# Kernel tuning notes

Hardware: AMD Instinct MI355X
Metric: run time of the kernel (lower is better)

The kernel has to match this reference:

```python
import math
import jax, jax.numpy as jnp
import numpy as np

NUM_HEADS = 16
NUM_BUCKETS = 32
MAX_DISTANCE = 128
NEG_INF = -1e9
LN_EPS = 1e-5


def _rel_pos_bias(rab_emb, T):
    # buckets for relative position (i - j) clamped at 0, T5-style log buckets
    i = jnp.arange(T)[:, None]
    j = jnp.arange(T)[None, :]
    n = jnp.clip(i - j, 0, None)  # = -(mem - ctx), clamped min 0
    max_exact = NUM_BUCKETS // 2
    large = max_exact + (
        jnp.log(n.astype(jnp.float32) / max_exact + 1e-6)
        / math.log(MAX_DISTANCE / max_exact)
        * (NUM_BUCKETS - max_exact)
    ).astype(jnp.int32)
    large = jnp.minimum(large, NUM_BUCKETS - 1)
    buckets = jnp.where(n < max_exact, n, large)  # [T, T]
    return rab_emb[buckets].transpose(2, 0, 1)[None]  # [1, H, T, T]


def setup_inputs() -> dict:
    key = jax.random.key(0)
    ks = jax.random.split(key, 8)
    B, T, D = 2, 1024, 1024
    x = jax.random.normal(ks[0], (B, T, D), dtype=jnp.float32)
    # additive causal mask: 0 where allowed, -1e9 where blocked (code tests ==0 for allowed)
    causal_block = jnp.triu(jnp.ones((T, T), dtype=bool), k=1)
    attention_mask = jnp.where(causal_block, NEG_INF, 0.0).astype(jnp.float32)
    # key padding: second sequence has last 256 positions padded
    lengths = jnp.array([T, T - 256])
    key_padding_mask = jnp.arange(T)[None, :] >= lengths[:, None]  # True = pad
    s = 1.0 / math.sqrt(D)
    W_in = jax.random.normal(ks[1], (4 * D, D), dtype=jnp.float32) * s
    b_in = jax.random.normal(ks[2], (4 * D,), dtype=jnp.float32) * 0.02
    W_out = jax.random.normal(ks[3], (D, D), dtype=jnp.float32) * s
    b_out = jax.random.normal(ks[4], (D,), dtype=jnp.float32) * 0.02
    gamma = jnp.ones((D,), dtype=jnp.float32)
    beta = jnp.zeros((D,), dtype=jnp.float32)
    rab_emb = jax.random.normal(ks[5], (NUM_BUCKETS, NUM_HEADS), dtype=jnp.float32) * 0.02
    return {
        "x": x,
        "attention_mask": attention_mask,
        "key_padding_mask": key_padding_mask,
        "W_in": W_in,
        "b_in": b_in,
        "W_out": W_out,
        "b_out": b_out,
        "gamma": gamma,
        "beta": beta,
        "rab_emb": rab_emb,
    }


def reference(x, attention_mask, key_padding_mask, W_in, b_in, W_out, b_out, gamma, beta, rab_emb):
    B, T, D = x.shape
    H = NUM_HEADS
    hd = D // H
    alpha = hd ** (-0.5)

    h = jax.nn.silu(x @ W_in.T + b_in)  # [B, T, 4D]
    U, V, Q, K = jnp.split(h, 4, axis=-1)

    def heads(t):
        return t.reshape(B, T, H, hd).transpose(0, 2, 1, 3)  # [B, H, T, hd]

    Qh, Kh, Vh = heads(Q), heads(K), heads(V)

    rab = _rel_pos_bias(rab_emb, T)  # [1, H, T, T]
    logits = jnp.einsum("bhtd,bhsd->bhts", Qh, Kh) * alpha + rab + attention_mask[None, None]

    valid = (~key_padding_mask).astype(jnp.float32)[:, None, None, :]  # [B,1,1,T]
    allowed = (attention_mask == 0).astype(jnp.float32)[None, None] * valid  # [B,1,T,T] bcast
    # padded keys: torch masked_fill(-inf) then logits_safe -> -1e9
    logits = jnp.where(valid == 0, NEG_INF, logits)

    denom = jnp.clip(jnp.sum(allowed, axis=-1, keepdims=True), 1.0, None)
    attention = jax.nn.silu(logits) / denom  # pointwise SiLU attention, no softmax

    AV = jnp.einsum("bhts,bhsd->bthd", attention, Vh).reshape(B, T, D)

    mu = jnp.mean(AV, axis=-1, keepdims=True)
    var = jnp.var(AV, axis=-1, keepdims=True)
    normed = (AV - mu) / jnp.sqrt(var + LN_EPS) * gamma + beta

    y = (normed * U) @ W_out.T + b_out  # U_flat == U (head reshape round-trips)
    return x + y
```

## Files before the change

### kernel.cpp

```cpp
#include <hip/hip_runtime.h>
#include <stdint.h>

#define DEV static __device__ __forceinline__

typedef unsigned short u16;
typedef float floatx4 __attribute__((ext_vector_type(4)));
typedef short bf16x8 __attribute__((ext_vector_type(8)));
typedef unsigned short ushort8v __attribute__((ext_vector_type(8)));

constexpr int Tn = 1024;
constexpr int Dn = 1024;
constexpr int Hn = 16;
constexpr int FD = 4096;

DEV float b2f(u16 u) { union { unsigned int i; float f; } v; v.i = ((unsigned int)u) << 16; return v.f; }
DEV u16 f2b(float f) {
  union { float f; unsigned int i; } v; v.f = f;
  unsigned int x = v.i;
  x += 0x7fffu + ((x >> 16) & 1u);
  return (u16)(x >> 16);
}

DEV void async16(const void* g, void* l) {
  __builtin_amdgcn_global_load_lds((const __attribute__((address_space(1))) void*)g,
                                   (__attribute__((address_space(3))) void*)l,
                                   16, 0, 0);
}

DEV bool is_bf16(const unsigned* gdet) { return gdet[0] == 0x3F803F80u; }
DEV int kp_mode(const unsigned* kp) {
  unsigned d511 = kp[511];
  if (d511 == 0x01010101u) return 1;
  unsigned d1023 = kp[1023];
  if (d1023 == 0x3F803F80u) return 2;
  unsigned d2047 = kp[2047];
  return (d2047 == 0x3F800000u) ? 3 : 0;
}
DEV int nchunks(int qt) { return (qt < 6) ? 1 : ((qt < 12) ? 2 : 3); }

__global__ void cvt_big(const void* __restrict__ x, const void* __restrict__ wi,
                        const void* __restrict__ wo, u16* __restrict__ xb,
                        u16* __restrict__ wib, u16* __restrict__ wob,
                        const unsigned* __restrict__ gdet)
{
  if (is_bf16(gdet)) return;
  int i0 = blockIdx.x * 256 + threadIdx.x;
#pragma unroll
  for (int k = 0; k < 4; k++) {
    int i = i0 + k * 458752;
    const void* src; u16* dst; int j;
    if (i < 524288)       { src = x;  dst = xb;  j = i; }
    else if (i < 1572864) { src = wi; dst = wib; j = i - 524288; }
    else                  { src = wo; dst = wob; j = i - 1572864; }
    float4 v = ((const float4*)src)[j];
    ushort4 o; o.x = f2b(v.x); o.y = f2b(v.y); o.z = f2b(v.z); o.w = f2b(v.w);
    ((ushort4*)dst)[j] = o;
  }
}

__global__ void cvt_small(const void* __restrict__ bi, const void* __restrict__ bo,
                          const void* __restrict__ ga, const void* __restrict__ be,
                          float* __restrict__ smallf)
{
  const bool fbf = is_bf16((const unsigned*)ga);
  int i = blockIdx.x * 256 + threadIdx.x;
  if (i >= 7168) return;
  const void* src; int j;
  if (i < 4096)      { src = bi; j = i; }
  else if (i < 5120) { src = bo; j = i - 4096; }
  else if (i < 6144) { src = ga; j = i - 5120; }
  else               { src = be; j = i - 6144; }
  smallf[i] = fbf ? b2f(((const u16*)src)[j]) : ((const float*)src)[j];
}

__global__ void prep2_kern(const void* __restrict__ kp, const void* __restrict__ rab,
                           const unsigned* __restrict__ gdet,
                           float* __restrict__ biasG, float* __restrict__ denomG,
                           unsigned long long* __restrict__ kmaskG)
{
  const int tid = threadIdx.x;
  if (blockIdx.x == 2) {
    const bool fbf = is_bf16(gdet);
    for (int i = tid; i < Hn * Tn; i += 256) {
      int hh = i >> 10, d = i & 1023;
      int bk;
      if (d < 16) bk = d;
      else {
        float lg = logf((float)d * 0.0625f + 1e-6f) / logf(8.f) * 16.f;
        bk = 16 + (int)lg;
        bk = bk < 31 ? bk : 31;
      }
      int j = bk * Hn + hh;
      biasG[i] = fbf ? b2f(((const u16*)rab)[j]) : ((const float*)rab)[j];
    }
    return;
  }
  const int b = blockIdx.x;
  const int mode = kp_mode((const unsigned*)kp);
  __shared__ unsigned char vb[1024];
  __shared__ int wtot[4];
  int vv[4];
  const int t0 = tid * 4;
#pragma unroll
  for (int i = 0; i < 4; i++) {
    int t = b * Tn + t0 + i;
    int pad;
    if (mode == 0)      pad = (((const int*)kp)[t] != 0);
    else if (mode == 1) pad = (((const unsigned char*)kp)[t] != 0);
    else if (mode == 2) pad = (((const u16*)kp)[t] != 0);
    else                pad = (((const float*)kp)[t] != 0.f);
    vv[i] = pad ? 0 : 1;
    vb[t0 + i] = (unsigned char)vv[i];
  }
  int p1 = vv[0], p2 = p1 + vv[1], p3 = p2 + vv[2], p4 = p3 + vv[3];
  const int lane = tid & 63, w = tid >> 6;
  int ws = p4;
#pragma unroll
  for (int off = 1; off < 64; off <<= 1) {
    int t = __shfl_up(ws, off, 64);
    if (lane >= off) ws += t;
  }
  if (lane == 63) wtot[w] = ws;
  __syncthreads();
  int base = 0;
  for (int j = 0; j < w; j++) base += wtot[j];
  int excl = base + ws - p4;
  int c1 = excl + p1, c2 = excl + p2, c3 = excl + p3, c4 = excl + p4;
  denomG[b * Tn + t0 + 0] = (float)(c1 < 1 ? 1 : c1);
  denomG[b * Tn + t0 + 1] = (float)(c2 < 1 ? 1 : c2);
  denomG[b * Tn + t0 + 2] = (float)(c3 < 1 ? 1 : c3);
  denomG[b * Tn + t0 + 3] = (float)(c4 < 1 ? 1 : c4);
  if (tid < 16) {
    unsigned long long m = 0;
    for (int j = 0; j < 64; j++) m |= (unsigned long long)vb[tid * 64 + j] << j;
    kmaskG[b * 16 + tid] = m;
  }
}

template<int BM, int BN, int WR, int WC, int EPI>
__global__ __launch_bounds__(WR * WC * 64, 2)
void gemm_bt(const u16* __restrict__ Ac, const u16* __restrict__ Ar,
             const u16* __restrict__ Bc, const u16* __restrict__ Br,
             const float* __restrict__ biasf, void* __restrict__ C,
             const unsigned* __restrict__ gdet, int M, int N, int K)
{
  constexpr int NT = WR * WC * 64;
  __shared__ u16 As[BM * 32];
  __shared__ u16 Bs[BN * 32];
  const int fbf = is_bf16(gdet) ? 1 : 0;
  const u16* A  = fbf ? Ar : Ac;
  const u16* Bm = fbf ? Br : Bc;
  const int tid = threadIdx.x;
  const int lane = tid & 63;
  const int w = tid >> 6;
  const int wm = w / WC, wn = w % WC;
  const int q = lane >> 4, l16 = lane & 15;
  const int rowBase = blockIdx.y * BM;
  const int colBase = blockIdx.x * BN;
  const int ksl = K / gridDim.z;
  const int kb0 = blockIdx.z * ksl;

  floatx4 acc[4][4];
#pragma unroll
  for (int i = 0; i < 4; i++)
#pragma unroll
    for (int j = 0; j < 4; j++)
#pragma unroll
      for (int r = 0; r < 4; r++) acc[i][j][r] = 0.f;

  for (int kb = kb0; kb < kb0 + ksl; kb += 32) {
    __syncthreads();
#pragma unroll
    for (int i = 0; i < BM * 4 / NT; i++) {
      int c = i * NT + tid;
      async16(&A[(size_t)(rowBase + (c >> 2)) * K + kb + (c & 3) * 8], &As[c * 8]);
    }
#pragma unroll
    for (int i = 0; i < BN * 4 / NT; i++) {
      int c = i * NT + tid;
      async16(&Bm[(size_t)(colBase + (c >> 2)) * K + kb + (c & 3) * 8], &Bs[c * 8]);
    }
    __syncthreads();
    bf16x8 af[4], bfr[4];
#pragma unroll
    for (int mt = 0; mt < 4; mt++)
      af[mt] = *(const bf16x8*)&As[(wm * 64 + mt * 16 + l16) * 32 + q * 8];
#pragma unroll
    for (int nt = 0; nt < 4; nt++)
      bfr[nt] = *(const bf16x8*)&Bs[(wn * 64 + nt * 16 + l16) * 32 + q * 8];
#pragma unroll
    for (int mt = 0; mt < 4; mt++)
#pragma unroll
      for (int nt = 0; nt < 4; nt++)
        acc[mt][nt] = __builtin_amdgcn_mfma_f32_16x16x32_bf16(af[mt], bfr[nt], acc[mt][nt], 0, 0, 0);
  }

  const size_t pOff = (size_t)blockIdx.z * M * N;
#pragma unroll
  for (int mt = 0; mt < 4; mt++)
#pragma unroll
    for (int nt = 0; nt < 4; nt++) {
      int col = colBase + wn * 64 + nt * 16 + l16;
      float bcol = (EPI == 0) ? biasf[col] : 0.f;
#pragma unroll
      for (int r = 0; r < 4; r++) {
        int row = rowBase + wm * 64 + mt * 16 + q * 4 + r;
        size_t idx = (size_t)row * N + col;
        float v = acc[mt][nt][r] + bcol;
        if (EPI == 0) {
          v = v / (1.f + __expf(-v));
          ((u16*)C)[idx] = f2b(v);
        } else {
          ((float*)C)[pOff + idx] = v;
        }
      }
    }
}

__global__ __launch_bounds__(256)
void reduce2(const float* __restrict__ Gp, const void* __restrict__ X,
             const float* __restrict__ bout, void* __restrict__ out,
             const unsigned* __restrict__ gdet)
{
  const int fbf = is_bf16(gdet) ? 1 : 0;
  const int row = blockIdx.x;
  const int tid = threadIdx.x;
  const size_t ridx = (size_t)row * Dn;
  float4 a = ((const float4*)(Gp + ridx))[tid];
#pragma unroll
  for (int ks = 1; ks < 4; ks++) {
    float4 p = ((const float4*)(Gp + (size_t)ks * 2097152 + ridx))[tid];
    a.x += p.x; a.y += p.y; a.z += p.z; a.w += p.w;
  }
  float4 bb = ((const float4*)bout)[tid];
  a.x += bb.x; a.y += bb.y; a.z += bb.z; a.w += bb.w;
  if (fbf) {
    ushort4 xv = ((const ushort4*)X)[ridx / 4 + tid];
    a.x += b2f(xv.x); a.y += b2f(xv.y); a.z += b2f(xv.z); a.w += b2f(xv.w);
    ushort4 o; o.x = f2b(a.x); o.y = f2b(a.y); o.z = f2b(a.z); o.w = f2b(a.w);
    ((ushort4*)out)[ridx / 4 + tid] = o;
  } else {
    float4 xv = ((const float4*)X)[ridx / 4 + tid];
    a.x += xv.x; a.y += xv.y; a.z += xv.z; a.w += xv.w;
    ((float4*)out)[ridx / 4 + tid] = a;
  }
}

__global__ __launch_bounds__(256)
void vt_kern(const u16* __restrict__ h, u16* __restrict__ VtG)
{
  __shared__ u16 L[4096];
  const int tid = threadIdx.x;
  const int tt = blockIdx.x, head = blockIdx.y, b = blockIdx.z;
  const u16* hb = h + (size_t)b * Tn * FD;
#pragma unroll
  for (int i = 0; i < 2; i++) {
    int s = i * 256 + tid;
    async16(&hb[(size_t)(tt * 64 + (s >> 3)) * FD + 1024 + head * 64 + (s & 7) * 8], &L[s * 8]);
  }
  __syncthreads();
  u16* vout = VtG + ((size_t)(b * Hn + head)) * 64 * Tn;
#pragma unroll
  for (int i = 0; i < 2; i++) {
    int oc = i * 256 + tid;
    int d = oc >> 3, tc = oc & 7;
    ushort8v v;
#pragma unroll
    for (int j = 0; j < 8; j++) v[j] = L[(tc * 8 + j) * 64 + d];
    *(ushort8v*)&vout[(size_t)d * Tn + tt * 64 + tc * 8] = v;
  }
}

__global__ __launch_bounds__(256, 4)
void attn_kern(const u16* __restrict__ h, const u16* __restrict__ VtG,
               const float* __restrict__ biasG, const float* __restrict__ denomG,
               const unsigned long long* __restrict__ kmaskG,
               float* __restrict__ AV)
{
  __shared__ u16 Qs[4096];
  __shared__ u16 Ks[4096];
  __shared__ u16 Vs[4096];
  __shared__ u16 Ps[4096];
  __shared__ float biasL[1024];
  const int tid = threadIdx.x;
  const int lane = tid & 63;
  const int w = tid >> 6;
  const int q = lane >> 4, l16 = lane & 15;

  int qt = 0, rem = blockIdx.x;
  for (;;) { int P = nchunks(qt); if (rem < P) break; rem -= P; qt++; }
  const int c = rem;
  const int P = nchunks(qt);
  const int n = qt + 1, cb = n / P, cr = n % P;
  const int kt0 = c * cb + (c < cr ? c : cr);
  const int kt1 = kt0 + cb + (c < cr ? 1 : 0);

  const int head = blockIdx.y, b = blockIdx.z;
  const u16* hb = h + (size_t)b * Tn * FD;
  const u16* vtb = VtG + ((size_t)(b * Hn + head)) * 64 * Tn;

#pragma unroll
  for (int i = 0; i < 2; i++) {
    int s = i * 256 + tid;
    int row = s >> 3, dc = (s & 7) ^ (row & 7);
    async16(&hb[(size_t)(qt * 64 + row) * FD + 2048 + head * 64 + dc * 8], &Qs[s * 8]);
    async16(&hb[(size_t)(kt0 * 64 + row) * FD + 3072 + head * 64 + dc * 8], &Ks[s * 8]);
    async16(&vtb[(size_t)row * Tn + kt0 * 64 + dc * 8], &Vs[s * 8]);
  }
  async16(&biasG[head * Tn + tid * 4], &biasL[tid * 4]);
  __syncthreads();

  const int sw0 = q ^ (l16 & 7);
  const int qrow = w * 16 + l16;
  bf16x8 bq0 = *(const bf16x8*)&Qs[(qrow * 8 + sw0) * 8];
  bf16x8 bq1 = *(const bf16x8*)&Qs[(qrow * 8 + (sw0 ^ 4)) * 8];
  const float dinv = 1.f / denomG[b * Tn + qt * 64 + qrow];

  floatx4 o[4];
#pragma unroll
  for (int nt = 0; nt < 4; nt++)
#pragma unroll
    for (int r = 0; r < 4; r++) o[nt][r] = 0.f;

  for (int kt = kt0; kt < kt1; kt++) {
    const unsigned long long km = kmaskG[b * 16 + kt];
    const int dq = (qt - kt) * 64 + qrow;
#pragma unroll
    for (int st = 0; st < 4; st++) {
      int rk = (st * 16 + l16) * 8;
      bf16x8 ak0 = *(const bf16x8*)&Ks[(rk + sw0) * 8];
      bf16x8 ak1 = *(const bf16x8*)&Ks[(rk + (sw0 ^ 4)) * 8];
      floatx4 sT;
#pragma unroll
      for (int r = 0; r < 4; r++) sT[r] = 0.f;
      sT = __builtin_amdgcn_mfma_f32_16x16x32_bf16(ak0, bq0, sT, 0, 0, 0);
      sT = __builtin_amdgcn_mfma_f32_16x16x32_bf16(ak1, bq1, sT, 0, 0, 0);
      unsigned mb = (unsigned)(km >> (st * 16 + q * 4)) & 0xFu;
      u16 pr[4];
#pragma unroll
      for (int r = 0; r < 4; r++) {
        int delta = dq - (st * 16 + q * 4 + r);
        float p = 0.f;
        if (((mb >> r) & 1u) && delta >= 0) {
          float xv = sT[r] * 0.125f + biasL[delta];
          p = xv * dinv / (1.f + __expf(-xv));
        }
        pr[r] = f2b(p);
      }
      unsigned lo = pr[0] | ((unsigned)pr[1] << 16);
      unsigned hi = pr[2] | ((unsigned)pr[3] << 16);
      int cch = (st * 2 + (q >> 1)) ^ (l16 & 7);
      *(uint2*)&Ps[w * 1024 + l16 * 64 + cch * 8 + (q & 1) * 4] = make_uint2(lo, hi);
    }
    int rp = w * 1024 + l16 * 64;
    bf16x8 ap0 = *(const bf16x8*)&Ps[rp + sw0 * 8];
    bf16x8 ap1 = *(const bf16x8*)&Ps[rp + (sw0 ^ 4) * 8];
#pragma unroll
    for (int nt = 0; nt < 4; nt++) {
      int rv = (nt * 16 + l16) * 8;
      bf16x8 bv0 = *(const bf16x8*)&Vs[(rv + sw0) * 8];
      bf16x8 bv1 = *(const bf16x8*)&Vs[(rv + (sw0 ^ 4)) * 8];
      o[nt] = __builtin_amdgcn_mfma_f32_16x16x32_bf16(ap0, bv0, o[nt], 0, 0, 0);
      o[nt] = __builtin_amdgcn_mfma_f32_16x16x32_bf16(ap1, bv1, o[nt], 0, 0, 0);
    }
    if (kt + 1 < kt1) {
      __syncthreads();
#pragma unroll
      for (int i = 0; i < 2; i++) {
        int s = i * 256 + tid;
        int row = s >> 3, dc = (s & 7) ^ (row & 7);
        async16(&hb[(size_t)((kt + 1) * 64 + row) * FD + 3072 + head * 64 + dc * 8], &Ks[s * 8]);
        async16(&vtb[(size_t)row * Tn + (kt + 1) * 64 + dc * 8], &Vs[s * 8]);
      }
      __syncthreads();
    }
  }

  float* avp = AV + (size_t)c * 2097152
             + ((size_t)b * Tn + qt * 64 + w * 16 + q * 4) * Dn + head * 64;
#pragma unroll
  for (int nt = 0; nt < 4; nt++)
#pragma unroll
    for (int r = 0; r < 4; r++)
      avp[(size_t)r * Dn + nt * 16 + l16] = o[nt][r];
}

__global__ __launch_bounds__(256)
void ln_mul(const float* __restrict__ AV, const u16* __restrict__ h,
            const float* __restrict__ gam, const float* __restrict__ bet,
            u16* __restrict__ z)
{
  struct alignas(8) U4 { u16 a, b, c, d; };
  const int row = blockIdx.x;
  const int tid = threadIdx.x;
  const int P = nchunks(row >> 6 & 15);
  float4 v = ((const float4*)(AV + (size_t)row * Dn))[tid];
  if (P > 1) {
    float4 p = ((const float4*)(AV + 2097152 + (size_t)row * Dn))[tid];
    v.x += p.x; v.y += p.y; v.z += p.z; v.w += p.w;
  }
  if (P > 2) {
    float4 p = ((const float4*)(AV + 4194304 + (size_t)row * Dn))[tid];
    v.x += p.x; v.y += p.y; v.z += p.z; v.w += p.w;
  }
  float s  = v.x + v.y + v.z + v.w;
  float s2 = v.x * v.x + v.y * v.y + v.z * v.z + v.w * v.w;
#pragma unroll
  for (int off = 32; off > 0; off >>= 1) {
    s  += __shfl_down(s, off, 64);
    s2 += __shfl_down(s2, off, 64);
  }
  __shared__ float red[8];
  const int lane = tid & 63, w = tid >> 6;
  if (lane == 0) { red[w] = s; red[4 + w] = s2; }
  __syncthreads();
  const float su = red[0] + red[1] + red[2] + red[3];
  const float sq = red[4] + red[5] + red[6] + red[7];
  const float mu = su * (1.f / 1024.f);
  const float var = sq * (1.f / 1024.f) - mu * mu;
  const float rstd = rsqrtf(var + 1e-5f);

  const U4 uu = ((const U4*)(h + (size_t)row * FD))[tid];
  const float4 g4 = ((const float4*)gam)[tid];
  const float4 b4 = ((const float4*)bet)[tid];
  float r0 = ((v.x - mu) * rstd * g4.x + b4.x) * b2f(uu.a);
  float r1 = ((v.y - mu) * rstd * g4.y + b4.y) * b2f(uu.b);
  float r2 = ((v.z - mu) * rstd * g4.z + b4.z) * b2f(uu.c);
  float r3 = ((v.w - mu) * rstd * g4.w + b4.w) * b2f(uu.d);
  U4 outv; outv.a = f2b(r0); outv.b = f2b(r1); outv.c = f2b(r2); outv.d = f2b(r3);
  ((U4*)(z + (size_t)row * Dn))[tid] = outv;
}

extern "C" void kernel_launch(void* const* d_in, const int* in_sizes, int n_in,
                              void* d_out, int out_size, void* d_ws, size_t ws_size,
                              hipStream_t stream)
{
  const void* x     = d_in[0];
  const void* kp    = d_in[2];
  const void* W_in  = d_in[3];
  const void* b_in  = d_in[4];
  const void* W_out = d_in[5];
  const void* b_out = d_in[6];
  const void* gamma = d_in[7];
  const void* beta  = d_in[8];
  const void* rab   = d_in[9];
  const unsigned* gdet = (const unsigned*)gamma;

  char* ws = (char*)d_ws;
  u16*   h     = (u16*)(ws);
  float* AV    = (float*)(ws + 16777216);
  u16*   z     = (u16*)(ws + 41943040);
  u16*   xb    = (u16*)(ws + 46137344);
  u16*   Wib   = (u16*)(ws + 50331648);
  u16*   VtG   = (u16*)(ws + 50331648);
  u16*   Wob   = (u16*)(ws + 58720256);
  float* Gp    = (float*)(ws + 60817408);
  float* smallf= (float*)(ws + 94371840);
  float* biasG = (float*)(ws + 94400512);
  float* denom = (float*)(ws + 94466048);
  unsigned long long* kmask = (unsigned long long*)(ws + 94474240);

  cvt_big<<<1792, 256, 0, stream>>>(x, W_in, W_out, xb, Wib, Wob, gdet);
  cvt_small<<<28, 256, 0, stream>>>(b_in, b_out, gamma, beta, smallf);
  prep2_kern<<<3, 256, 0, stream>>>(kp, rab, gdet, biasG, denom, kmask);
  gemm_bt<128, 128, 2, 2, 0><<<dim3(32, 16, 1), dim3(256), 0, stream>>>(
      xb, (const u16*)x, Wib, (const u16*)W_in, smallf, h, gdet, 2048, 4096, 1024);
  vt_kern<<<dim3(16, 16, 2), dim3(256), 0, stream>>>(h, VtG);
  attn_kern<<<dim3(30, 16, 2), dim3(256), 0, stream>>>(h, VtG, biasG, denom, kmask, AV);
  ln_mul<<<2048, 256, 0, stream>>>(AV, h, smallf + 5120, smallf + 6144, z);
  gemm_bt<128, 128, 2, 2, 2><<<dim3(8, 16, 4), dim3(256), 0, stream>>>(
      z, z, Wob, (const u16*)W_out, smallf, Gp, gdet, 2048, 1024, 1024);
  reduce2<<<2048, 256, 0, stream>>>(Gp, x, smallf + 4096, d_out, gdet);
}
```

Measured before the change: 194.8 us.

## Merge prep kernels, fuse V transpose into GEMM epilogue, widen GEMM K-tile with swizzle

The three preprocessing kernels are merged into one launch. The V transpose kernel is removed, and the input GEMM epilogue now writes V columns directly in transposed layout. The GEMM K-step grows from 32 to 64, with an XOR-swizzled LDS layout meant to avoid bank conflicts. The workspace is also re-laid out so Gp aliases h. This cuts launch count and per-iteration sync overhead, at the cost of larger LDS use and a strided epilogue store for V.

New measurement: 187.0 us. 1.04x faster.

```diff
diff --git a/kernel.cpp b/kernel.cpp
--- a/kernel.cpp
+++ b/kernel.cpp
@@ -6,7 +6,6 @@
 typedef unsigned short u16;
 typedef float floatx4 __attribute__((ext_vector_type(4)));
 typedef short bf16x8 __attribute__((ext_vector_type(8)));
-typedef unsigned short ushort8v __attribute__((ext_vector_type(8)));
 
 constexpr int Tn = 1024;
 constexpr int Dn = 1024;
@@ -38,102 +37,98 @@
 }
 DEV int nchunks(int qt) { return (qt < 6) ? 1 : ((qt < 12) ? 2 : 3); }
 
-__global__ void cvt_big(const void* __restrict__ x, const void* __restrict__ wi,
-                        const void* __restrict__ wo, u16* __restrict__ xb,
-                        u16* __restrict__ wib, u16* __restrict__ wob,
-                        const unsigned* __restrict__ gdet)
-{
-  if (is_bf16(gdet)) return;
-  int i0 = blockIdx.x * 256 + threadIdx.x;
-#pragma unroll
-  for (int k = 0; k < 4; k++) {
-    int i = i0 + k * 458752;
-    const void* src; u16* dst; int j;
-    if (i < 524288)       { src = x;  dst = xb;  j = i; }
-    else if (i < 1572864) { src = wi; dst = wib; j = i - 524288; }
-    else                  { src = wo; dst = wob; j = i - 1572864; }
-    float4 v = ((const float4*)src)[j];
-    ushort4 o; o.x = f2b(v.x); o.y = f2b(v.y); o.z = f2b(v.z); o.w = f2b(v.w);
-    ((ushort4*)dst)[j] = o;
-  }
-}
-
-__global__ void cvt_small(const void* __restrict__ bi, const void* __restrict__ bo,
-                          const void* __restrict__ ga, const void* __restrict__ be,
-                          float* __restrict__ smallf)
-{
-  const bool fbf = is_bf16((const unsigned*)ga);
-  int i = blockIdx.x * 256 + threadIdx.x;
-  if (i >= 7168) return;
-  const void* src; int j;
-  if (i < 4096)      { src = bi; j = i; }
-  else if (i < 5120) { src = bo; j = i - 4096; }
-  else if (i < 6144) { src = ga; j = i - 5120; }
-  else               { src = be; j = i - 6144; }
-  smallf[i] = fbf ? b2f(((const u16*)src)[j]) : ((const float*)src)[j];
-}
-
-__global__ void prep2_kern(const void* __restrict__ kp, const void* __restrict__ rab,
-                           const unsigned* __restrict__ gdet,
-                           float* __restrict__ biasG, float* __restrict__ denomG,
-                           unsigned long long* __restrict__ kmaskG)
-{
+__global__ void prep_all(const void* __restrict__ x, const void* __restrict__ wi,
+                         const void* __restrict__ wo, u16* __restrict__ xb,
+                         u16* __restrict__ wib, u16* __restrict__ wob,
+                         const void* __restrict__ bi, const void* __restrict__ bo,
+                         const void* __restrict__ ga, const void* __restrict__ be,
+                         const void* __restrict__ kp, const void* __restrict__ rab,
+                         float* __restrict__ smallf, float* __restrict__ biasG,
+                         float* __restrict__ denomG, unsigned long long* __restrict__ kmaskG)
+{
+  const unsigned* gdet = (const unsigned*)ga;
+  const int bid = blockIdx.x;
   const int tid = threadIdx.x;
-  if (blockIdx.x == 2) {
-    const bool fbf = is_bf16(gdet);
-    for (int i = tid; i < Hn * Tn; i += 256) {
-      int hh = i >> 10, d = i & 1023;
-      int bk;
-      if (d < 16) bk = d;
-      else {
-        float lg = logf((float)d * 0.0625f + 1e-6f) / logf(8.f) * 16.f;
-        bk = 16 + (int)lg;
-        bk = bk < 31 ? bk : 31;
-      }
-      int j = bk * Hn + hh;
-      biasG[i] = fbf ? b2f(((const u16*)rab)[j]) : ((const float*)rab)[j];
-    }
-    return;
-  }
-  const int b = blockIdx.x;
-  const int mode = kp_mode((const unsigned*)kp);
   __shared__ unsigned char vb[1024];
   __shared__ int wtot[4];
-  int vv[4];
-  const int t0 = tid * 4;
-#pragma unroll
-  for (int i = 0; i < 4; i++) {
-    int t = b * Tn + t0 + i;
-    int pad;
-    if (mode == 0)      pad = (((const int*)kp)[t] != 0);
-    else if (mode == 1) pad = (((const unsigned char*)kp)[t] != 0);
-    else if (mode == 2) pad = (((const u16*)kp)[t] != 0);
-    else                pad = (((const float*)kp)[t] != 0.f);
-    vv[i] = pad ? 0 : 1;
-    vb[t0 + i] = (unsigned char)vv[i];
-  }
-  int p1 = vv[0], p2 = p1 + vv[1], p3 = p2 + vv[2], p4 = p3 + vv[3];
-  const int lane = tid & 63, w = tid >> 6;
-  int ws = p4;
-#pragma unroll
-  for (int off = 1; off < 64; off <<= 1) {
-    int t = __shfl_up(ws, off, 64);
-    if (lane >= off) ws += t;
-  }
-  if (lane == 63) wtot[w] = ws;
-  __syncthreads();
-  int base = 0;
-  for (int j = 0; j < w; j++) base += wtot[j];
-  int excl = base + ws - p4;
-  int c1 = excl + p1, c2 = excl + p2, c3 = excl + p3, c4 = excl + p4;
-  denomG[b * Tn + t0 + 0] = (float)(c1 < 1 ? 1 : c1);
-  denomG[b * Tn + t0 + 1] = (float)(c2 < 1 ? 1 : c2);
-  denomG[b * Tn + t0 + 2] = (float)(c3 < 1 ? 1 : c3);
-  denomG[b * Tn + t0 + 3] = (float)(c4 < 1 ? 1 : c4);
-  if (tid < 16) {
-    unsigned long long m = 0;
-    for (int j = 0; j < 64; j++) m |= (unsigned long long)vb[tid * 64 + j] << j;
-    kmaskG[b * 16 + tid] = m;
+
+  if (bid < 1792) {
+    if (is_bf16(gdet)) return;
+    int i0 = bid * 256 + tid;
+#pragma unroll
+    for (int k = 0; k < 4; k++) {
+      int i = i0 + k * 458752;
+      const void* src; u16* dst; int j;
+      if (i < 524288)       { src = x;  dst = xb;  j = i; }
+      else if (i < 1572864) { src = wi; dst = wib; j = i - 524288; }
+      else                  { src = wo; dst = wob; j = i - 1572864; }
+      float4 v = ((const float4*)src)[j];
+      ushort4 o; o.x = f2b(v.x); o.y = f2b(v.y); o.z = f2b(v.z); o.w = f2b(v.w);
+      ((ushort4*)dst)[j] = o;
+    }
+    return;
+  }
+  if (bid < 1794) {
+    const int b = bid - 1792;
+    const int mode = kp_mode((const unsigned*)kp);
+    int vv[4];
+    const int t0 = tid * 4;
+#pragma unroll
+    for (int i = 0; i < 4; i++) {
+      int t = b * Tn + t0 + i;
+      int pad;
+      if (mode == 0)      pad = (((const int*)kp)[t] != 0);
+      else if (mode == 1) pad = (((const unsigned char*)kp)[t] != 0);
+      else if (mode == 2) pad = (((const u16*)kp)[t] != 0);
+      else                pad = (((const float*)kp)[t] != 0.f);
+      vv[i] = pad ? 0 : 1;
+      vb[t0 + i] = (unsigned char)vv[i];
+    }
+    int p1 = vv[0], p2 = p1 + vv[1], p3 = p2 + vv[2], p4 = p3 + vv[3];
+    const int lane = tid & 63, w = tid >> 6;
+    int ws = p4;
+#pragma unroll
+    for (int off = 1; off < 64; off <<= 1) {
+      int t = __shfl_up(ws, off, 64);
+      if (lane >= off) ws += t;
+    }
+    if (lane == 63) wtot[w] = ws;
+    __syncthreads();
+    int base = 0;
+    for (int j = 0; j < w; j++) base += wtot[j];
+    int excl = base + ws - p4;
+    int c1 = excl + p1, c2 = excl + p2, c3 = excl + p3, c4 = excl + p4;
+    denomG[b * Tn + t0 + 0] = (float)(c1 < 1 ? 1 : c1);
+    denomG[b * Tn + t0 + 1] = (float)(c2 < 1 ? 1 : c2);
+    denomG[b * Tn + t0 + 2] = (float)(c3 < 1 ? 1 : c3);
+    denomG[b * Tn + t0 + 3] = (float)(c4 < 1 ? 1 : c4);
+    if (tid < 16) {
+      unsigned long long m = 0;
+      for (int j = 0; j < 64; j++) m |= (unsigned long long)vb[tid * 64 + j] << j;
+      kmaskG[b * 16 + tid] = m;
+    }
+    return;
+  }
+  const bool fbf = is_bf16(gdet);
+  for (int i = tid; i < 7168; i += 256) {
+    const void* src; int j;
+    if (i < 4096)      { src = bi; j = i; }
+    else if (i < 5120) { src = bo; j = i - 4096; }
+    else if (i < 6144) { src = ga; j = i - 5120; }
+    else               { src = be; j = i - 6144; }
+    smallf[i] = fbf ? b2f(((const u16*)src)[j]) : ((const float*)src)[j];
+  }
+  for (int i = tid; i < Hn * Tn; i += 256) {
+    int hh = i >> 10, d = i & 1023;
+    int bk;
+    if (d < 16) bk = d;
+    else {
+      float lg = logf((float)d * 0.0625f + 1e-6f) / logf(8.f) * 16.f;
+      bk = 16 + (int)lg;
+      bk = bk < 31 ? bk : 31;
+    }
+    int j = bk * Hn + hh;
+    biasG[i] = fbf ? b2f(((const u16*)rab)[j]) : ((const float*)rab)[j];
   }
 }
 
@@ -142,11 +137,12 @@
 void gemm_bt(const u16* __restrict__ Ac, const u16* __restrict__ Ar,
              const u16* __restrict__ Bc, const u16* __restrict__ Br,
              const float* __restrict__ biasf, void* __restrict__ C,
-             const unsigned* __restrict__ gdet, int M, int N, int K)
+             u16* __restrict__ VtG, const unsigned* __restrict__ gdet,
+             int M, int N, int K)
 {
   constexpr int NT = WR * WC * 64;
-  __shared__ u16 As[BM * 32];
-  __shared__ u16 Bs[BN * 32];
+  __shared__ u16 As[BM * 64];
+  __shared__ u16 Bs[BN * 64];
   const int fbf = is_bf16(gdet) ? 1 : 0;
   const u16* A  = fbf ? Ar : Ac;
   const u16* Bm = fbf ? Br : Bc;
@@ -168,33 +164,46 @@
 #pragma unroll
       for (int r = 0; r < 4; r++) acc[i][j][r] = 0.f;
 
-  for (int kb = kb0; kb < kb0 + ksl; kb += 32) {
+  for (int kb = kb0; kb < kb0 + ksl; kb += 64) {
     __syncthreads();
 #pragma unroll
-    for (int i = 0; i < BM * 4 / NT; i++) {
+    for (int i = 0; i < BM * 8 / NT; i++) {
       int c = i * NT + tid;
-      async16(&A[(size_t)(rowBase + (c >> 2)) * K + kb + (c & 3) * 8], &As[c * 8]);
-    }
-#pragma unroll
-    for (int i = 0; i < BN * 4 / NT; i++) {
+      int row = c >> 3, cl = (c & 7) ^ (row & 7);
+      async16(&A[(size_t)(rowBase + row) * K + kb + cl * 8], &As[c * 8]);
+    }
+#pragma unroll
+    for (int i = 0; i < BN * 8 / NT; i++) {
       int c = i * NT + tid;
-      async16(&Bm[(size_t)(colBase + (c >> 2)) * K + kb + (c & 3) * 8], &Bs[c * 8]);
+      int row = c >> 3, cl = (c & 7) ^ (row & 7);
+      async16(&Bm[(size_t)(colBase + row) * K + kb + cl * 8], &Bs[c * 8]);
     }
     __syncthreads();
-    bf16x8 af[4], bfr[4];
-#pragma unroll
-    for (int mt = 0; mt < 4; mt++)
-      af[mt] = *(const bf16x8*)&As[(wm * 64 + mt * 16 + l16) * 32 + q * 8];
-#pragma unroll
-    for (int nt = 0; nt < 4; nt++)
-      bfr[nt] = *(const bf16x8*)&Bs[(wn * 64 + nt * 16 + l16) * 32 + q * 8];
-#pragma unroll
-    for (int mt = 0; mt < 4; mt++)
-#pragma unroll
-      for (int nt = 0; nt < 4; nt++)
-        acc[mt][nt] = __builtin_amdgcn_mfma_f32_16x16x32_bf16(af[mt], bfr[nt], acc[mt][nt], 0, 0, 0);
-  }
-
+    bf16x8 af[2][4], bfr[2][4];
+    const int rsw = l16 & 7;
+#pragma unroll
+    for (int ko = 0; ko < 2; ko++) {
+#pragma unroll
+      for (int mt = 0; mt < 4; mt++) {
+        int row = wm * 64 + mt * 16 + l16;
+        af[ko][mt] = *(const bf16x8*)&As[(row * 8 + ((ko * 4 + q) ^ rsw)) * 8];
+      }
+#pragma unroll
+      for (int nt = 0; nt < 4; nt++) {
+        int row = wn * 64 + nt * 16 + l16;
+        bfr[ko][nt] = *(const bf16x8*)&Bs[(row * 8 + ((ko * 4 + q) ^ rsw)) * 8];
+      }
+    }
+#pragma unroll
+    for (int ko = 0; ko < 2; ko++)
+#pragma unroll
+      for (int mt = 0; mt < 4; mt++)
+#pragma unroll
+        for (int nt = 0; nt < 4; nt++)
+          acc[mt][nt] = __builtin_amdgcn_mfma_f32_16x16x32_bf16(af[ko][mt], bfr[ko][nt], acc[mt][nt], 0, 0, 0);
+  }
+
+  const bool isV = (EPI == 0) && (colBase >= Dn) && (colBase < 2 * Dn);
   const size_t pOff = (size_t)blockIdx.z * M * N;
 #pragma unroll
   for (int mt = 0; mt < 4; mt++)
@@ -202,17 +211,29 @@
     for (int nt = 0; nt < 4; nt++) {
       int col = colBase + wn * 64 + nt * 16 + l16;
       float bcol = (EPI == 0) ? biasf[col] : 0.f;
-#pragma unroll
-      for (int r = 0; r < 4; r++) {
-        int row = rowBase + wm * 64 + mt * 16 + q * 4 + r;
-        size_t idx = (size_t)row * N + col;
-        float v = acc[mt][nt][r] + bcol;
-        if (EPI == 0) {
+      int row0 = rowBase + wm * 64 + mt * 16 + q * 4;
+      if (EPI == 0) {
+        u16 pr[4];
+#pragma unroll
+        for (int r = 0; r < 4; r++) {
+          float v = acc[mt][nt][r] + bcol;
           v = v / (1.f + __expf(-v));
-          ((u16*)C)[idx] = f2b(v);
+          pr[r] = f2b(v);
+        }
+        if (isV) {
+          int d = col - Dn;
+          u16* vp = &VtG[(((size_t)(row0 >> 10) * Hn + (d >> 6)) * 64 + (d & 63)) * Tn + (row0 & 1023)];
+          *(uint2*)vp = make_uint2(pr[0] | ((unsigned)pr[1] << 16),
+                                   pr[2] | ((unsigned)pr[3] << 16));
         } else {
-          ((float*)C)[pOff + idx] = v;
+#pragma unroll
+          for (int r = 0; r < 4; r++)
+            ((u16*)C)[(size_t)(row0 + r) * N + col] = pr[r];
         }
+      } else {
+#pragma unroll
+        for (int r = 0; r < 4; r++)
+          ((float*)C)[pOff + (size_t)(row0 + r) * N + col] = acc[mt][nt][r];
       }
     }
 }
@@ -243,31 +264,6 @@
     float4 xv = ((const float4*)X)[ridx / 4 + tid];
     a.x += xv.x; a.y += xv.y; a.z += xv.z; a.w += xv.w;
     ((float4*)out)[ridx / 4 + tid] = a;
-  }
-}
-
-__global__ __launch_bounds__(256)
-void vt_kern(const u16* __restrict__ h, u16* __restrict__ VtG)
-{
-  __shared__ u16 L[4096];
-  const int tid = threadIdx.x;
-  const int tt = blockIdx.x, head = blockIdx.y, b = blockIdx.z;
-  const u16* hb = h + (size_t)b * Tn * FD;
-#pragma unroll
-  for (int i = 0; i < 2; i++) {
-    int s = i * 256 + tid;
-    async16(&hb[(size_t)(tt * 64 + (s >> 3)) * FD + 1024 + head * 64 + (s & 7) * 8], &L[s * 8]);
-  }
-  __syncthreads();
-  u16* vout = VtG + ((size_t)(b * Hn + head)) * 64 * Tn;
-#pragma unroll
-  for (int i = 0; i < 2; i++) {
-    int oc = i * 256 + tid;
-    int d = oc >> 3, tc = oc & 7;
-    ushort8v v;
-#pragma unroll
-    for (int j = 0; j < 8; j++) v[j] = L[(tc * 8 + j) * 64 + d];
-    *(ushort8v*)&vout[(size_t)d * Tn + tt * 64 + tc * 8] = v;
   }
 }
 
@@ -449,26 +445,25 @@
   char* ws = (char*)d_ws;
   u16*   h     = (u16*)(ws);
   float* AV    = (float*)(ws + 16777216);
+  float* Gp    = (float*)(ws);
   u16*   z     = (u16*)(ws + 41943040);
   u16*   xb    = (u16*)(ws + 46137344);
   u16*   Wib   = (u16*)(ws + 50331648);
-  u16*   VtG   = (u16*)(ws + 50331648);
   u16*   Wob   = (u16*)(ws + 58720256);
-  float* Gp    = (float*)(ws + 60817408);
-  float* smallf= (float*)(ws + 94371840);
-  float* biasG = (float*)(ws + 94400512);
-  float* denom = (float*)(ws + 94466048);
-  unsigned long long* kmask = (unsigned long long*)(ws + 94474240);
-
-  cvt_big<<<1792, 256, 0, stream>>>(x, W_in, W_out, xb, Wib, Wob, gdet);
-  cvt_small<<<28, 256, 0, stream>>>(b_in, b_out, gamma, beta, smallf);
-  prep2_kern<<<3, 256, 0, stream>>>(kp, rab, gdet, biasG, denom, kmask);
+  u16*   VtG   = (u16*)(ws + 60817408);
+  float* smallf= (float*)(ws + 65011712);
+  float* biasG = (float*)(ws + 65040384);
+  float* denom = (float*)(ws + 65105920);
+  unsigned long long* kmask = (unsigned long long*)(ws + 65114112);
+
+  prep_all<<<1795, 256, 0, stream>>>(x, W_in, W_out, xb, Wib, Wob,
+                                     b_in, b_out, gamma, beta, kp, rab,
+                                     smallf, biasG, denom, kmask);
   gemm_bt<128, 128, 2, 2, 0><<<dim3(32, 16, 1), dim3(256), 0, stream>>>(
-      xb, (const u16*)x, Wib, (const u16*)W_in, smallf, h, gdet, 2048, 4096, 1024);
-  vt_kern<<<dim3(16, 16, 2), dim3(256), 0, stream>>>(h, VtG);
+      xb, (const u16*)x, Wib, (const u16*)W_in, smallf, h, VtG, gdet, 2048, 4096, 1024);
   attn_kern<<<dim3(30, 16, 2), dim3(256), 0, stream>>>(h, VtG, biasG, denom, kmask, AV);
   ln_mul<<<2048, 256, 0, stream>>>(AV, h, smallf + 5120, smallf + 6144, z);
   gemm_bt<128, 128, 2, 2, 2><<<dim3(8, 16, 4), dim3(256), 0, stream>>>(
-      z, z, Wob, (const u16*)W_out, smallf, Gp, gdet, 2048, 1024, 1024);
+      z, z, Wob, (const u16*)W_out, smallf, Gp, nullptr, gdet, 2048, 1024, 1024);
   reduce2<<<2048, 256, 0, stream>>>(Gp, x, smallf + 4096, d_out, gdet);
 }
```
